# Performance work log

Measured on AMD Instinct MI355X. Metric: run time of the kernel, lower is better.

## Reference

```python
import jax, jax.numpy as jnp
import numpy as np

B, N, K, CIN, COUT = 8, 65536, 16, 3, 64


def setup_inputs() -> dict:
    key = jax.random.key(0)
    k1, k2, k3 = jax.random.split(key, 3)
    return {
        "x": jax.random.normal(k1, (B, N, CIN), dtype=jnp.float32),
        "kernel_points": jax.random.normal(k2, (K, 3), dtype=jnp.float32),
        "weights": jax.random.normal(k3, (K, CIN, COUT), dtype=jnp.float32),
        "sigma": jnp.float32(1.0),
    }


def reference(x, kernel_points, weights, sigma):
    # squared distance from each point to each kernel point: [B, N, K]
    diff = x[:, :, None, :] - kernel_points[None, None, :, :]  # [B, N, K, 3]
    d2 = jnp.sum(diff * diff, axis=-1)
    g = jnp.exp(-0.5 * d2 / (sigma * sigma))  # gaussian correlation [B, N, K]
    # out[b,n,o] = sum_k g[b,n,k] * sum_i x[b,n,i] * W[k,i,o]
    return jnp.einsum("bnk,bni,kio->bno", g, x, weights)
```

## Files before the change

kernel.cpp:

```cpp
#include <hip/hip_runtime.h>


typedef __bf16  bf16x8 __attribute__((ext_vector_type(8)));
typedef float   f32x4  __attribute__((ext_vector_type(4)));
typedef unsigned int   u32x4  __attribute__((ext_vector_type(4)));

union OctU {
    unsigned short s[8];
    u32x4          u4;
    bf16x8         v;
};

__device__ __forceinline__ unsigned short f2bf(float f) {
    unsigned u = __builtin_bit_cast(unsigned, f);
    u += 0x7FFFu + ((u >> 16) & 1u);
    return (unsigned short)(u >> 16);
}

__global__ __launch_bounds__(256) void kpconv_mfma(
    const float* __restrict__ x,
    const float* __restrict__ kp,
    const float* __restrict__ w,
    const float* __restrict__ sigma,
    float* __restrict__ out)
{
    __shared__ u32x4 ldsA[2304];

    const int tid  = threadIdx.x;
    const int lane = tid & 63;
    const int wv   = tid >> 6;
    const int q    = lane >> 4;
    const int n16  = lane & 15;
    const long long base = (long long)blockIdx.x * 256;

    bf16x8 bfrag[2][4];
#pragma unroll
    for (int h = 0; h < 2; ++h) {
#pragma unroll
        for (int ot = 0; ot < 4; ++ot) {
            OctU o;
#pragma unroll
            for (int j = 0; j < 8; ++j) {
                int kk = h * 32 + q * 8 + j;
                float v = (kk < 48) ? w[kk * 64 + ot * 16 + n16] : 0.0f;
                o.s[j] = f2bf(v);
            }
            bfrag[h][ot] = o.v;
        }
    }

    {
        const float sg = sigma[0];
        const float scale = -0.72134752f / (sg * sg);
        const long long p = base + tid;
        float xv[3];
        xv[0] = x[p * 3 + 0];
        xv[1] = x[p * 3 + 1];
        xv[2] = x[p * 3 + 2];
        float g[16];
#pragma unroll
        for (int k = 0; k < 16; ++k) {
            float dx = xv[0] - kp[k * 3 + 0];
            float dy = xv[1] - kp[k * 3 + 1];
            float dz = xv[2] - kp[k * 3 + 2];
            float d2 = dx * dx + dy * dy + dz * dz;
            g[k] = exp2f(d2 * scale);
        }
        const int tile = tid >> 4;
        const int m    = tid & 15;
#pragma unroll
        for (int o = 0; o < 8; ++o) {
            OctU ou;
#pragma unroll
            for (int j8 = 0; j8 < 8; ++j8) {
                int j = o * 8 + j8;
                ou.s[j8] = (j < 48) ? f2bf(g[j / 3] * xv[j % 3])
                                    : (unsigned short)0;
            }
            int chunk = tile * 128 + (o >> 2) * 64 + (o & 3) * 16 + m;
            ldsA[chunk + (chunk >> 3)] = ou.u4;
        }
    }
    __syncthreads();

#pragma unroll
    for (int t4 = 0; t4 < 4; ++t4) {
        const int t  = wv * 4 + t4;
        const int c0 = t * 128 + q * 16 + n16;
        const int c1 = c0 + 64;
        OctU a0u, a1u;
        a0u.u4 = ldsA[c0 + (c0 >> 3)];
        a1u.u4 = ldsA[c1 + (c1 >> 3)];
        f32x4 acc[4];
#pragma unroll
        for (int ot = 0; ot < 4; ++ot) {
            acc[ot] = (f32x4){0.f, 0.f, 0.f, 0.f};
            acc[ot] = __builtin_amdgcn_mfma_f32_16x16x32_bf16(a0u.v, bfrag[0][ot], acc[ot], 0, 0, 0);
            acc[ot] = __builtin_amdgcn_mfma_f32_16x16x32_bf16(a1u.v, bfrag[1][ot], acc[ot], 0, 0, 0);
        }
        const long long prow = base + t * 16 + q * 4;
#pragma unroll
        for (int ot = 0; ot < 4; ++ot) {
#pragma unroll
            for (int r = 0; r < 4; ++r) {
                out[(prow + r) * 64 + ot * 16 + n16] = acc[ot][r];
            }
        }
    }
}

extern "C" void kernel_launch(void* const* d_in, const int* in_sizes, int n_in,
                              void* d_out, int out_size, void* d_ws, size_t ws_size,
                              hipStream_t stream) {
    const float* x     = (const float*)d_in[0];
    const float* kp    = (const float*)d_in[1];
    const float* w     = (const float*)d_in[2];
    const float* sigma = (const float*)d_in[3];
    float* out = (float*)d_out;

    const int npoints = in_sizes[0] / 3;
    const int blocks  = npoints / 256;
    kpconv_mfma<<<blocks, 256, 0, stream>>>(x, kp, w, sigma, out);
}
```

Before: 144.0 us.

## Build MFMA A fragments in registers directly, removing LDS staging and barrier

```diff
diff --git a/kernel.cpp b/kernel.cpp
--- a/kernel.cpp
+++ b/kernel.cpp
@@ -3,19 +3,8 @@
 
 typedef __bf16  bf16x8 __attribute__((ext_vector_type(8)));
 typedef float   f32x4  __attribute__((ext_vector_type(4)));
-typedef unsigned int   u32x4  __attribute__((ext_vector_type(4)));
 
-union OctU {
-    unsigned short s[8];
-    u32x4          u4;
-    bf16x8         v;
-};
-
-__device__ __forceinline__ unsigned short f2bf(float f) {
-    unsigned u = __builtin_bit_cast(unsigned, f);
-    u += 0x7FFFu + ((u >> 16) & 1u);
-    return (unsigned short)(u >> 16);
-}
+union OctU { unsigned short s[8]; bf16x8 v; };
 
 __global__ __launch_bounds__(256) void kpconv_mfma(
     const float* __restrict__ x,
@@ -24,14 +13,20 @@
     const float* __restrict__ sigma,
     float* __restrict__ out)
 {
-    __shared__ u32x4 ldsA[2304];
-
     const int tid  = threadIdx.x;
     const int lane = tid & 63;
     const int wv   = tid >> 6;
     const int q    = lane >> 4;
     const int n16  = lane & 15;
     const long long base = (long long)blockIdx.x * 256;
+
+    float kpt[4][3];
+#pragma unroll
+    for (int e = 0; e < 4; ++e) {
+        const int kpi = (e >> 1) * 8 + 2 * q + (e & 1);
+#pragma unroll
+        for (int d = 0; d < 3; ++d) kpt[e][d] = kp[kpi * 3 + d];
+    }
 
     bf16x8 bfrag[2][4];
 #pragma unroll
@@ -41,64 +36,58 @@
             OctU o;
 #pragma unroll
             for (int j = 0; j < 8; ++j) {
-                int kk = h * 32 + q * 8 + j;
-                float v = (kk < 48) ? w[kk * 64 + ot * 16 + n16] : 0.0f;
-                o.s[j] = f2bf(v);
+                float v = 0.0f;
+                if (j < 6) {
+                    const int kpi = h * 8 + 2 * q + (j >= 3);
+                    const int i   = (j >= 3) ? (j - 3) : j;
+                    v = w[(kpi * 3 + i) * 64 + ot * 16 + n16];
+                }
+                o.v[j] = (__bf16)v;
             }
             bfrag[h][ot] = o.v;
         }
     }
 
-    {
-        const float sg = sigma[0];
-        const float scale = -0.72134752f / (sg * sg);
-        const long long p = base + tid;
-        float xv[3];
-        xv[0] = x[p * 3 + 0];
-        xv[1] = x[p * 3 + 1];
-        xv[2] = x[p * 3 + 2];
-        float g[16];
+    const float sg = sigma[0];
+    const float scale = -0.72134752f / (sg * sg);
+
+    float xv[4][3];
 #pragma unroll
-        for (int k = 0; k < 16; ++k) {
-            float dx = xv[0] - kp[k * 3 + 0];
-            float dy = xv[1] - kp[k * 3 + 1];
-            float dz = xv[2] - kp[k * 3 + 2];
-            float d2 = dx * dx + dy * dy + dz * dz;
-            g[k] = exp2f(d2 * scale);
-        }
-        const int tile = tid >> 4;
-        const int m    = tid & 15;
+    for (int t4 = 0; t4 < 4; ++t4) {
+        const long long p = base + wv * 64 + t4 * 16 + n16;
 #pragma unroll
-        for (int o = 0; o < 8; ++o) {
-            OctU ou;
-#pragma unroll
-            for (int j8 = 0; j8 < 8; ++j8) {
-                int j = o * 8 + j8;
-                ou.s[j8] = (j < 48) ? f2bf(g[j / 3] * xv[j % 3])
-                                    : (unsigned short)0;
-            }
-            int chunk = tile * 128 + (o >> 2) * 64 + (o & 3) * 16 + m;
-            ldsA[chunk + (chunk >> 3)] = ou.u4;
-        }
+        for (int d = 0; d < 3; ++d) xv[t4][d] = x[p * 3 + d];
     }
-    __syncthreads();
 
 #pragma unroll
     for (int t4 = 0; t4 < 4; ++t4) {
-        const int t  = wv * 4 + t4;
-        const int c0 = t * 128 + q * 16 + n16;
-        const int c1 = c0 + 64;
-        OctU a0u, a1u;
-        a0u.u4 = ldsA[c0 + (c0 >> 3)];
-        a1u.u4 = ldsA[c1 + (c1 >> 3)];
+        float g[4];
+#pragma unroll
+        for (int e = 0; e < 4; ++e) {
+            const float dx = xv[t4][0] - kpt[e][0];
+            const float dy = xv[t4][1] - kpt[e][1];
+            const float dz = xv[t4][2] - kpt[e][2];
+            g[e] = exp2f((dx * dx + dy * dy + dz * dz) * scale);
+        }
+        OctU a0, a1;
+#pragma unroll
+        for (int j = 0; j < 3; ++j) {
+            a0.v[j]     = (__bf16)(g[0] * xv[t4][j]);
+            a0.v[j + 3] = (__bf16)(g[1] * xv[t4][j]);
+            a1.v[j]     = (__bf16)(g[2] * xv[t4][j]);
+            a1.v[j + 3] = (__bf16)(g[3] * xv[t4][j]);
+        }
+        a0.v[6] = a0.v[7] = (__bf16)0.0f;
+        a1.v[6] = a1.v[7] = (__bf16)0.0f;
+
         f32x4 acc[4];
 #pragma unroll
         for (int ot = 0; ot < 4; ++ot) {
             acc[ot] = (f32x4){0.f, 0.f, 0.f, 0.f};
-            acc[ot] = __builtin_amdgcn_mfma_f32_16x16x32_bf16(a0u.v, bfrag[0][ot], acc[ot], 0, 0, 0);
-            acc[ot] = __builtin_amdgcn_mfma_f32_16x16x32_bf16(a1u.v, bfrag[1][ot], acc[ot], 0, 0, 0);
+            acc[ot] = __builtin_amdgcn_mfma_f32_16x16x32_bf16(a0.v, bfrag[0][ot], acc[ot], 0, 0, 0);
+            acc[ot] = __builtin_amdgcn_mfma_f32_16x16x32_bf16(a1.v, bfrag[1][ot], acc[ot], 0, 0, 0);
         }
-        const long long prow = base + t * 16 + q * 4;
+        const long long prow = base + wv * 64 + t4 * 16 + q * 4;
 #pragma unroll
         for (int ot = 0; ot < 4; ++ot) {
 #pragma unroll
```

After: 154.0 us. 6.9% more time.
